# Kernel optimization log

Hardware: AMD Instinct MI355X
Metric: run time of the kernel (lower is better)

Reference implementation:

```python
import jax, jax.numpy as jnp
import numpy as np

V, E, H, M, C = 50000, 300, 256, 512, 20  # vocab, emb_dim, hid_dim, max_dim, n_classes
S, B = 512, 64  # seq_len, batch


def setup_inputs() -> dict:
    key = jax.random.key(0)
    ks = jax.random.split(key, 16)
    s = lambda i, shape: jax.random.normal(ks[i], shape, dtype=jnp.float32) * 0.05
    return dict(
        inp=jax.random.randint(ks[0], (S, B), 0, V),
        emb_table=s(1, (V, E)),
        c_l0=s(2, (H,)), c_r0=s(3, (H,)),
        W_l_w=s(4, (H, H)), W_l_b=s(5, (H,)),
        W_r_w=s(6, (H, H)), W_r_b=s(7, (H,)),
        W_sl_w=s(8, (H, E)), W_sl_b=s(9, (H,)),
        W_sr_w=s(10, (H, E)), W_sr_b=s(11, (H,)),
        max_w=s(12, (M, 2 * H + E)), max_b=s(13, (M,)),
        doc_w=s(14, (C, M)), doc_b=s(15, (C,)),
    )


def reference(inp, emb_table, c_l0, c_r0, W_l_w, W_l_b, W_r_w, W_r_b,
              W_sl_w, W_sl_b, W_sr_w, W_sr_b, max_w, max_b, doc_w, doc_b):
    emb = emb_table[inp]  # [S, B, E]
    # precomputed per-token projections (batched once, as in the original)
    emb_ls = jnp.einsum('sbe,he->sbh', emb, W_sl_w) + W_sl_b  # [S, B, H]
    emb_rs = jnp.einsum('sbe,he->sbh', emb, W_sr_w) + W_sr_b  # [S, B, H]

    batch = inp.shape[1]

    def make_step(W, b):
        def step(c, x):  # c: [B, H], x: [B, H]
            c = jnp.tanh(c @ W.T + b + x)
            return c, c
        return step

    c0_l = jnp.broadcast_to(c_l0, (batch, c_l0.shape[0]))
    c0_r = jnp.broadcast_to(c_r0, (batch, c_r0.shape[0]))
    _, c_ls = jax.lax.scan(make_step(W_l_w, W_l_b), c0_l, emb_ls)          # left-to-right
    _, c_rs = jax.lax.scan(make_step(W_r_w, W_r_b), c0_r, emb_rs[::-1])    # right-to-left
    c_rs = c_rs[::-1]  # re-align to original time order (stack(c_rs[::-1]))

    cat = jnp.concatenate([c_ls, emb, c_rs], axis=-1)  # [S, B, 2H+E]
    y = jnp.tanh(jnp.einsum('sbc,mc->sbm', cat, max_w) + max_b)  # [S, B, M]
    y_max = jnp.max(y, axis=0)  # [B, M] element-wise max-pool over time
    return jax.nn.log_softmax(y_max @ doc_w.T + doc_b, axis=-1)  # [B, C]
```

## Files before the change

### kernel.cpp

```cpp
#include <hip/hip_runtime.h>
#include <hip/hip_bf16.h>

constexpr int kS = 512;
constexpr int kB = 64;
constexpr int kE = 300;
constexpr int kH = 256;
constexpr int kM = 512;
constexpr int kC = 20;

typedef short s16x8 __attribute__((ext_vector_type(8)));
typedef float f32x4 __attribute__((ext_vector_type(4)));
typedef unsigned short u16x4 __attribute__((ext_vector_type(4)));
typedef _Float16 f16x8 __attribute__((ext_vector_type(8)));

__device__ __forceinline__ float fast_tanh(float z) {
    z = fminf(15.f, fmaxf(-15.f, z));
    float e = __expf(2.f * z);
    return 1.f - 2.f / (e + 1.f);
}

__device__ __forceinline__ unsigned short f2bf(float f) {
    __hip_bfloat16 h = __float2bfloat16(f);
    return *(unsigned short*)&h;
}
__device__ __forceinline__ float bf2f(unsigned short u) {
    __hip_bfloat16 h = *(__hip_bfloat16*)&u;
    return __bfloat162float(h);
}
union F16U { _Float16 h; unsigned short u; };
__device__ __forceinline__ unsigned short f16bits(_Float16 h) { F16U x; x.h = h; return x.u; }


__global__ __launch_bounds__(256) void prepw_kernel(
    const float* __restrict__ max_w,
    const float* __restrict__ wsl, const float* __restrict__ wsr,
    const float* __restrict__ wl, const float* __restrict__ wr,
    unsigned short* __restrict__ Wmax, unsigned short* __restrict__ Wproj,
    unsigned short* __restrict__ Wscan)
{
    int idx = blockIdx.x * 256 + threadIdx.x;
    if (idx < 512 * 832) {
        int r = idx / 832, c = idx - r * 832;
        float v;
        if (c < 556)      v = max_w[r * 812 + c];
        else if (c < 576) v = 0.f;
        else              v = max_w[r * 812 + (c - 20)];
        Wmax[idx] = f2bf(v);
    }
    if (idx < 512 * 320) {
        int r = idx / 320, c = idx - r * 320;
        float v = 0.f;
        if (c < 300) v = (r < 256) ? wsl[r * 300 + c] : wsr[(r - 256) * 300 + c];
        Wproj[idx] = f2bf(v);
    }
    if (idx < 2 * 256 * 256) {
        int d = idx >> 16, rc = idx & 65535;
        float v = (d ? wr : wl)[rc];
        Wscan[idx] = f16bits((_Float16)v);
    }
}

__global__ __launch_bounds__(128) void gather_kernel(
    const int* __restrict__ inp, const float* __restrict__ emb_table,
    unsigned short* __restrict__ E)
{
    const int row = blockIdx.x;
    const int b = row >> 9, s = row & 511;
    const int t = threadIdx.x;
    unsigned short* dst = E + (size_t)row * 320;
    const int v = inp[s * kB + b];
    const float* src = emb_table + (size_t)v * kE;
    if (t < 75) {
        float4 f = *(const float4*)&src[t * 4];
        u16x4 o = { f2bf(f.x), f2bf(f.y), f2bf(f.z), f2bf(f.w) };
        *(u16x4*)&dst[t * 4] = o;
    } else if (t < 80) {
        u16x4 z = { 0, 0, 0, 0 };
        *(u16x4*)&dst[300 + (t - 75) * 4] = z;
    }
}

__global__ __launch_bounds__(256) void proj_mfma_kernel(
    const unsigned short* __restrict__ E,
    const unsigned short* __restrict__ Wproj,
    const float* __restrict__ b_sl, const float* __restrict__ b_sr,
    unsigned short* __restrict__ XCL, unsigned short* __restrict__ XCR)
{
    __shared__ unsigned short As[128 * 40];
    __shared__ unsigned short Bs[128 * 40];
    const int tid = threadIdx.x;
    const int row0 = blockIdx.x * 128;
    const int col0 = blockIdx.y * 128;
    const int lane = tid & 63;
    const int wave = tid >> 6;
    const int wr = (wave >> 1) * 64, wc = (wave & 1) * 64;
    const int l15 = lane & 15, lk = (lane >> 4) * 8;
    const int srow = tid >> 1;
    const int sh = (tid & 1) * 16;

    const unsigned short* Ag = E + (size_t)(row0 + srow) * 320 + sh;
    const unsigned short* Bg = Wproj + (size_t)(col0 + srow) * 320 + sh;

    f32x4 acc[4][4] = {};
    float4 av0 = *(const float4*)Ag;
    float4 av1 = *(const float4*)(Ag + 8);
    float4 bv0 = *(const float4*)Bg;
    float4 bv1 = *(const float4*)(Bg + 8);

    for (int kk = 0; kk < 10; ++kk) {
        __syncthreads();
        *(float4*)&As[srow * 40 + sh] = av0;
        *(float4*)&As[srow * 40 + sh + 8] = av1;
        *(float4*)&Bs[srow * 40 + sh] = bv0;
        *(float4*)&Bs[srow * 40 + sh + 8] = bv1;
        __syncthreads();
        if (kk < 9) {
            av0 = *(const float4*)(Ag + (kk + 1) * 32);
            av1 = *(const float4*)(Ag + (kk + 1) * 32 + 8);
            bv0 = *(const float4*)(Bg + (kk + 1) * 32);
            bv1 = *(const float4*)(Bg + (kk + 1) * 32 + 8);
        }
        s16x8 af[4], bf[4];
#pragma unroll
        for (int f = 0; f < 4; ++f) {
            af[f] = *(const s16x8*)&As[(wr + f * 16 + l15) * 40 + lk];
            bf[f] = *(const s16x8*)&Bs[(wc + f * 16 + l15) * 40 + lk];
        }
#pragma unroll
        for (int i = 0; i < 4; ++i)
#pragma unroll
            for (int j = 0; j < 4; ++j)
                acc[i][j] = __builtin_amdgcn_mfma_f32_16x16x32_bf16(af[i], bf[j], acc[i][j], 0, 0, 0);
    }

    const int rbase = row0 + wr + (lane >> 4) * 4;
#pragma unroll
    for (int j = 0; j < 4; ++j) {
        const int col = col0 + wc + j * 16 + l15;
        const float bias = (col < kH) ? b_sl[col] : b_sr[col - kH];
        unsigned short* X = (col < kH) ? XCL : XCR;
        const int ccol = col & 255;
#pragma unroll
        for (int i = 0; i < 4; ++i) {
#pragma unroll
            for (int r = 0; r < 4; ++r) {
                const int row = rbase + i * 16 + r;
                const int s = row & 511, b = row >> 9;
                X[((size_t)s * 64 + b) * 256 + ccol] = f2bf(acc[i][j][r] + bias);
            }
        }
    }
}

__global__ __launch_bounds__(512, 2) void scan_mfma_kernel(
    const float* __restrict__ c_l0, const float* __restrict__ c_r0,
    const float* __restrict__ b_l, const float* __restrict__ b_r,
    const unsigned short* __restrict__ Wscan,
    unsigned short* __restrict__ XCL, unsigned short* __restrict__ XCR)
{
    __shared__ unsigned short cF[2][16 * 256];

    const int dir = blockIdx.x >> 2;
    const int bg  = blockIdx.x & 3;
    const int tid = threadIdx.x;
    const int lane = tid & 63;
    const int wave = tid >> 6;
    const int l15 = lane & 15;
    const int q4  = lane >> 4;
    const int lk  = q4 * 8;
    const int n0  = wave * 32;

    const float* bias = dir ? b_r : b_l;
    const float* c0v  = dir ? c_r0 : c_l0;
    const unsigned short* W = Wscan + (dir << 16);
    unsigned short* XC = dir ? XCR : XCL;

    f16x8 wf[2][8];
#pragma unroll
    for (int j = 0; j < 2; ++j)
#pragma unroll
        for (int ks = 0; ks < 8; ++ks)
            wf[j][ks] = *(const f16x8*)&W[(n0 + j * 16 + l15) * 256 + ks * 32 + lk];

    float biasv[2];
#pragma unroll
    for (int j = 0; j < 2; ++j) biasv[j] = bias[n0 + j * 16 + l15];

    unsigned short* xbase[4];
#pragma unroll
    for (int r = 0; r < 4; ++r)
        xbase[r] = XC + (size_t)(bg * 16 + q4 * 4 + r) * 256 + n0 + l15;

    int ridx[8], widx[2][4];
#pragma unroll
    for (int ks = 0; ks < 8; ++ks)
        ridx[ks] = (l15 * 256 + ks * 32 + lk) ^ ((l15 & 7) << 3);
#pragma unroll
    for (int j = 0; j < 2; ++j)
#pragma unroll
        for (int r = 0; r < 4; ++r) {
            int row = q4 * 4 + r;
            widx[j][r] = (row * 256 + n0 + j * 16 + l15) ^ ((row & 7) << 3);
        }

    if (tid < 256) {
        unsigned short hb = f16bits((_Float16)c0v[tid]);
        for (int row = 0; row < 16; ++row)
            cF[0][(row * 256 + tid) ^ ((row & 7) << 3)] = hb;
    }

    const int s0i = dir ? 511 : 0;
    const int s1i = dir ? 510 : 1;
    unsigned short xa[8], xb[8];
#pragma unroll
    for (int j = 0; j < 2; ++j)
#pragma unroll
        for (int r = 0; r < 4; ++r) {
            xa[j * 4 + r] = xbase[r][(size_t)s0i * 16384 + j * 16];
            xb[j * 4 + r] = xbase[r][(size_t)s1i * 16384 + j * 16];
        }
    __syncthreads();

    auto body = [&](int t, unsigned short (&xc)[8]) {
        const int st = dir ? (511 - t) : t;
        int sld = dir ? (st - 2) : (st + 2);
        sld = min(511, max(0, sld));
        const int p = t & 1;

        f32x4 acc[2];
#pragma unroll
        for (int j = 0; j < 2; ++j)
#pragma unroll
            for (int r = 0; r < 4; ++r)
                acc[j][r] = biasv[j] + bf2f(xc[j * 4 + r]);

#pragma unroll
        for (int j = 0; j < 2; ++j)
#pragma unroll
            for (int r = 0; r < 4; ++r)
                xc[j * 4 + r] = xbase[r][(size_t)sld * 16384 + j * 16];

        f16x8 ah[8];
#pragma unroll
        for (int ks = 0; ks < 8; ++ks)
            ah[ks] = *(const f16x8*)&cF[p][ridx[ks]];
#pragma unroll
        for (int ks = 0; ks < 8; ++ks) {
            acc[0] = __builtin_amdgcn_mfma_f32_16x16x32_f16(ah[ks], wf[0][ks], acc[0], 0, 0, 0);
            acc[1] = __builtin_amdgcn_mfma_f32_16x16x32_f16(ah[ks], wf[1][ks], acc[1], 0, 0, 0);
        }

#pragma unroll
        for (int j = 0; j < 2; ++j)
#pragma unroll
            for (int r = 0; r < 4; ++r) {
                float c = fast_tanh(acc[j][r]);
                xbase[r][(size_t)st * 16384 + j * 16] = f2bf(c);
                cF[p ^ 1][widx[j][r]] = f16bits((_Float16)c);
            }
        __syncthreads();
    };

    for (int t = 0; t < kS; t += 2) {
        body(t, xa);
        body(t + 1, xb);
    }
}

__global__ __launch_bounds__(256) void maxlayer_mfma_kernel(
    const unsigned short* __restrict__ XCL, const unsigned short* __restrict__ E,
    const unsigned short* __restrict__ XCR, const unsigned short* __restrict__ Wmax,
    float* __restrict__ part_max)
{
    __shared__ unsigned short As[128 * 40];
    __shared__ unsigned short Bs[128 * 40];
    __shared__ float red[2][128];
    const int tid = threadIdx.x;
    const int mt = blockIdx.x, sc = blockIdx.y, b = blockIdx.z;
    const int col0 = mt * 128;
    const int lane = tid & 63;
    const int wave = tid >> 6;
    const int wrow = wave >> 1;
    const int wr = wrow * 64, wc = (wave & 1) * 64;
    const int l15 = lane & 15, lk = (lane >> 4) * 8;
    const int srow = tid >> 1;
    const int sh = (tid & 1) * 16;

    const int s = sc * 128 + srow;
    const unsigned short* baseL = XCL + ((size_t)s * 64 + b) * 256 + sh;
    const unsigned short* baseE = E + (size_t)(b * 512 + s) * 320 + sh;
    const unsigned short* baseR = XCR + ((size_t)s * 64 + b) * 256 + sh;
    const unsigned short* Bg = Wmax + (size_t)(col0 + srow) * 832 + sh;

    auto aptr = [&](int kk) -> const unsigned short* {
        if (kk < 8)  return baseL + kk * 32;
        if (kk < 18) return baseE + (kk - 8) * 32;
        return baseR + (kk - 18) * 32;
    };

    f32x4 acc[4][4] = {};
    float4 av0 = *(const float4*)aptr(0);
    float4 av1 = *(const float4*)(aptr(0) + 8);
    float4 bv0 = *(const float4*)Bg;
    float4 bv1 = *(const float4*)(Bg + 8);

    for (int kk = 0; kk < 26; ++kk) {
        __syncthreads();
        *(float4*)&As[srow * 40 + sh] = av0;
        *(float4*)&As[srow * 40 + sh + 8] = av1;
        *(float4*)&Bs[srow * 40 + sh] = bv0;
        *(float4*)&Bs[srow * 40 + sh + 8] = bv1;
        __syncthreads();
        if (kk < 25) {
            const unsigned short* ap = aptr(kk + 1);
            av0 = *(const float4*)ap;
            av1 = *(const float4*)(ap + 8);
            bv0 = *(const float4*)(Bg + (kk + 1) * 32);
            bv1 = *(const float4*)(Bg + (kk + 1) * 32 + 8);
        }
        s16x8 af[4], bf[4];
#pragma unroll
        for (int f = 0; f < 4; ++f) {
            af[f] = *(const s16x8*)&As[(wr + f * 16 + l15) * 40 + lk];
            bf[f] = *(const s16x8*)&Bs[(wc + f * 16 + l15) * 40 + lk];
        }
#pragma unroll
        for (int i = 0; i < 4; ++i)
#pragma unroll
            for (int j = 0; j < 4; ++j)
                acc[i][j] = __builtin_amdgcn_mfma_f32_16x16x32_bf16(af[i], bf[j], acc[i][j], 0, 0, 0);
    }

#pragma unroll
    for (int j = 0; j < 4; ++j) {
        float m = -1e30f;
#pragma unroll
        for (int i = 0; i < 4; ++i)
#pragma unroll
            for (int r = 0; r < 4; ++r) m = fmaxf(m, acc[i][j][r]);
        m = fmaxf(m, __shfl_xor(m, 16));
        m = fmaxf(m, __shfl_xor(m, 32));
        if (lane < 16) red[wrow][wc + j * 16 + lane] = m;
    }
    __syncthreads();
    if (tid < 128) {
        float v = fmaxf(red[0][tid], red[1][tid]);
        part_max[((size_t)(b * 4 + sc)) * kM + col0 + tid] = v;
    }
}

__global__ __launch_bounds__(256) void final_kernel(
    const float* __restrict__ part_max, const float* __restrict__ max_b,
    const float* __restrict__ doc_w, const float* __restrict__ doc_b,
    float* __restrict__ out)
{
    const int b = blockIdx.x;
    const int t = threadIdx.x;
    __shared__ float ym[kM];
    __shared__ float red[160];
    __shared__ float logits[kC];

    for (int m = t; m < kM; m += 256) {
        float v = -1e30f;
        for (int ch = 0; ch < 4; ++ch)
            v = fmaxf(v, part_max[((size_t)(b * 4 + ch)) * kM + m]);
        ym[m] = fast_tanh(v + max_b[m]);
    }
    __syncthreads();
    if (t < 160) {
        int c = t >> 3, kg = t & 7;
        float s = 0.f;
        const float* wr = doc_w + c * kM + kg * 64;
        const float* yr = ym + kg * 64;
        for (int k = 0; k < 64; ++k) s += yr[k] * wr[k];
        red[t] = s;
    }
    __syncthreads();
    if (t < kC) {
        float s = doc_b[t];
        for (int kg = 0; kg < 8; ++kg) s += red[t * 8 + kg];
        logits[t] = s;
    }
    __syncthreads();
    if (t == 0) {
        float mx = logits[0];
        for (int c = 1; c < kC; ++c) mx = fmaxf(mx, logits[c]);
        float se = 0.f;
        for (int c = 0; c < kC; ++c) se += __expf(logits[c] - mx);
        float lse = mx + __logf(se);
        for (int c = 0; c < kC; ++c) out[b * kC + c] = logits[c] - lse;
    }
}

extern "C" void kernel_launch(void* const* d_in, const int* in_sizes, int n_in,
                              void* d_out, int out_size, void* d_ws, size_t ws_size,
                              hipStream_t stream) {
    const int* inp = (const int*)d_in[0];
    const float* emb_table = (const float*)d_in[1];
    const float* c_l0 = (const float*)d_in[2];
    const float* c_r0 = (const float*)d_in[3];
    const float* W_l_w = (const float*)d_in[4];
    const float* W_l_b = (const float*)d_in[5];
    const float* W_r_w = (const float*)d_in[6];
    const float* W_r_b = (const float*)d_in[7];
    const float* W_sl_w = (const float*)d_in[8];
    const float* W_sl_b = (const float*)d_in[9];
    const float* W_sr_w = (const float*)d_in[10];
    const float* W_sr_b = (const float*)d_in[11];
    const float* max_w = (const float*)d_in[12];
    const float* max_b = (const float*)d_in[13];
    const float* doc_w = (const float*)d_in[14];
    const float* doc_b = (const float*)d_in[15];
    float* out = (float*)d_out;

    char* w = (char*)d_ws;
    unsigned short* E     = (unsigned short*)(w);
    unsigned short* XCL   = (unsigned short*)(w + 20971520);
    unsigned short* XCR   = (unsigned short*)(w + 37748736);
    unsigned short* Wmax  = (unsigned short*)(w + 54525952);
    unsigned short* Wproj = (unsigned short*)(w + 55377920);
    float* part_max       = (float*)(w + 55705600);
    unsigned short* Wscan = (unsigned short*)(w + 56229888);

    prepw_kernel<<<(512 * 832 + 255) / 256, 256, 0, stream>>>(
        max_w, W_sl_w, W_sr_w, W_l_w, W_r_w, Wmax, Wproj, Wscan);
    gather_kernel<<<kS * kB, 128, 0, stream>>>(inp, emb_table, E);
    proj_mfma_kernel<<<dim3(256, 4), 256, 0, stream>>>(
        E, Wproj, W_sl_b, W_sr_b, XCL, XCR);
    scan_mfma_kernel<<<8, 512, 0, stream>>>(
        c_l0, c_r0, W_l_b, W_r_b, Wscan, XCL, XCR);
    maxlayer_mfma_kernel<<<dim3(4, 4, 64), 256, 0, stream>>>(
        XCL, E, XCR, Wmax, part_max);
    final_kernel<<<kB, 256, 0, stream>>>(part_max, max_b, doc_w, doc_b, out);
}
```

Baseline: 629.5 us.

## Transpose scan MFMA operands for packed stores and split accumulation chains

Swaps the A/B operands of the scan recurrence MFMA so each lane holds four consecutive hidden units. Global x loads and bf16 stores then become 8-byte vectorized accesses, and the LDS state write becomes a packed f16x4 store. The K loop is split into two independent accumulator chains to shorten the MFMA dependency latency on the serial critical path. Tanh now uses raw exp2/rcp intrinsics with packed conversions but without clamping, and the f16 conversion switches to round-toward-zero, which slightly changes numerics.

Measured after the change: 519.1 us. 1.21x faster.

```diff
diff --git a/kernel.cpp b/kernel.cpp
--- a/kernel.cpp
+++ b/kernel.cpp
@@ -12,6 +12,7 @@
 typedef float f32x4 __attribute__((ext_vector_type(4)));
 typedef unsigned short u16x4 __attribute__((ext_vector_type(4)));
 typedef _Float16 f16x8 __attribute__((ext_vector_type(8)));
+typedef __fp16 hf16x2 __attribute__((ext_vector_type(2)));
 
 __device__ __forceinline__ float fast_tanh(float z) {
     z = fminf(15.f, fmaxf(-15.f, z));
@@ -22,10 +23,6 @@
 __device__ __forceinline__ unsigned short f2bf(float f) {
     __hip_bfloat16 h = __float2bfloat16(f);
     return *(unsigned short*)&h;
-}
-__device__ __forceinline__ float bf2f(unsigned short u) {
-    __hip_bfloat16 h = *(__hip_bfloat16*)&u;
-    return __bfloat162float(h);
 }
 union F16U { _Float16 h; unsigned short u; };
 __device__ __forceinline__ unsigned short f16bits(_Float16 h) { F16U x; x.h = h; return x.u; }
@@ -167,7 +164,6 @@
     const int wave = tid >> 6;
     const int l15 = lane & 15;
     const int q4  = lane >> 4;
-    const int lk  = q4 * 8;
     const int n0  = wave * 32;
 
     const float* bias = dir ? b_r : b_l;
@@ -180,28 +176,24 @@
     for (int j = 0; j < 2; ++j)
 #pragma unroll
         for (int ks = 0; ks < 8; ++ks)
-            wf[j][ks] = *(const f16x8*)&W[(n0 + j * 16 + l15) * 256 + ks * 32 + lk];
-
-    float biasv[2];
-#pragma unroll
-    for (int j = 0; j < 2; ++j) biasv[j] = bias[n0 + j * 16 + l15];
-
-    unsigned short* xbase[4];
-#pragma unroll
-    for (int r = 0; r < 4; ++r)
-        xbase[r] = XC + (size_t)(bg * 16 + q4 * 4 + r) * 256 + n0 + l15;
-
-    int ridx[8], widx[2][4];
+            wf[j][ks] = *(const f16x8*)&W[(n0 + j * 16 + l15) * 256 + ks * 32 + q4 * 8];
+
+    float biasv[2][4];
+#pragma unroll
+    for (int j = 0; j < 2; ++j)
+#pragma unroll
+        for (int r = 0; r < 4; ++r)
+            biasv[j][r] = bias[n0 + j * 16 + q4 * 4 + r];
+
+    const unsigned int base0 = (unsigned)((bg * 16 + l15) * 256 + n0 + q4 * 4);
+
+    int ridx[8], widx[2];
 #pragma unroll
     for (int ks = 0; ks < 8; ++ks)
-        ridx[ks] = (l15 * 256 + ks * 32 + lk) ^ ((l15 & 7) << 3);
+        ridx[ks] = (l15 * 256 + ks * 32 + q4 * 8) ^ ((l15 & 7) << 3);
 #pragma unroll
     for (int j = 0; j < 2; ++j)
-#pragma unroll
-        for (int r = 0; r < 4; ++r) {
-            int row = q4 * 4 + r;
-            widx[j][r] = (row * 256 + n0 + j * 16 + l15) ^ ((row & 7) << 3);
-        }
+        widx[j] = (l15 * 256 + n0 + j * 16 + q4 * 4) ^ ((l15 & 7) << 3);
 
     if (tid < 256) {
         unsigned short hb = f16bits((_Float16)c0v[tid]);
@@ -211,53 +203,75 @@
 
     const int s0i = dir ? 511 : 0;
     const int s1i = dir ? 510 : 1;
-    unsigned short xa[8], xb[8];
-#pragma unroll
-    for (int j = 0; j < 2; ++j)
-#pragma unroll
-        for (int r = 0; r < 4; ++r) {
-            xa[j * 4 + r] = xbase[r][(size_t)s0i * 16384 + j * 16];
-            xb[j * 4 + r] = xbase[r][(size_t)s1i * 16384 + j * 16];
-        }
+    uint2 xa[2], xb[2];
+#pragma unroll
+    for (int j = 0; j < 2; ++j) {
+        xa[j] = *(const uint2*)(XC + base0 + (unsigned)s0i * 16384u + j * 16);
+        xb[j] = *(const uint2*)(XC + base0 + (unsigned)s1i * 16384u + j * 16);
+    }
     __syncthreads();
 
-    auto body = [&](int t, unsigned short (&xc)[8]) {
+    auto body = [&](int t, uint2 (&xc)[2]) {
         const int st = dir ? (511 - t) : t;
-        int sld = dir ? (st - 2) : (st + 2);
-        sld = min(511, max(0, sld));
+        const int sld = dir ? (st - 2 < 0 ? 0 : st - 2)
+                            : (st + 2 > 511 ? 511 : st + 2);
         const int p = t & 1;
 
-        f32x4 acc[2];
+        f32x4 acc[2], acc2[2];
+#pragma unroll
+        for (int j = 0; j < 2; ++j) {
+            const unsigned d0 = xc[j].x, d1 = xc[j].y;
+            acc[j][0] = biasv[j][0]; acc[j][1] = biasv[j][1];
+            acc[j][2] = biasv[j][2]; acc[j][3] = biasv[j][3];
+            acc2[j][0] = __uint_as_float(d0 << 16);
+            acc2[j][1] = __uint_as_float(d0 & 0xffff0000u);
+            acc2[j][2] = __uint_as_float(d1 << 16);
+            acc2[j][3] = __uint_as_float(d1 & 0xffff0000u);
+        }
+
 #pragma unroll
         for (int j = 0; j < 2; ++j)
-#pragma unroll
-            for (int r = 0; r < 4; ++r)
-                acc[j][r] = biasv[j] + bf2f(xc[j * 4 + r]);
-
-#pragma unroll
-        for (int j = 0; j < 2; ++j)
-#pragma unroll
-            for (int r = 0; r < 4; ++r)
-                xc[j * 4 + r] = xbase[r][(size_t)sld * 16384 + j * 16];
+            xc[j] = *(const uint2*)(XC + base0 + (unsigned)sld * 16384u + j * 16);
 
         f16x8 ah[8];
 #pragma unroll
         for (int ks = 0; ks < 8; ++ks)
             ah[ks] = *(const f16x8*)&cF[p][ridx[ks]];
 #pragma unroll
-        for (int ks = 0; ks < 8; ++ks) {
-            acc[0] = __builtin_amdgcn_mfma_f32_16x16x32_f16(ah[ks], wf[0][ks], acc[0], 0, 0, 0);
-            acc[1] = __builtin_amdgcn_mfma_f32_16x16x32_f16(ah[ks], wf[1][ks], acc[1], 0, 0, 0);
-        }
-
-#pragma unroll
-        for (int j = 0; j < 2; ++j)
-#pragma unroll
-            for (int r = 0; r < 4; ++r) {
-                float c = fast_tanh(acc[j][r]);
-                xbase[r][(size_t)st * 16384 + j * 16] = f2bf(c);
-                cF[p ^ 1][widx[j][r]] = f16bits((_Float16)c);
+        for (int ks = 0; ks < 4; ++ks) {
+            acc[0]  = __builtin_amdgcn_mfma_f32_16x16x32_f16(wf[0][ks],     ah[ks],     acc[0],  0, 0, 0);
+            acc[1]  = __builtin_amdgcn_mfma_f32_16x16x32_f16(wf[1][ks],     ah[ks],     acc[1],  0, 0, 0);
+            acc2[0] = __builtin_amdgcn_mfma_f32_16x16x32_f16(wf[0][ks + 4], ah[ks + 4], acc2[0], 0, 0, 0);
+            acc2[1] = __builtin_amdgcn_mfma_f32_16x16x32_f16(wf[1][ks + 4], ah[ks + 4], acc2[1], 0, 0, 0);
+        }
+
+#pragma unroll
+        for (int j = 0; j < 2; ++j) {
+            float t0, t1, t2, t3;
+            {
+                float z0 = acc[j][0] + acc2[j][0];
+                float z1 = acc[j][1] + acc2[j][1];
+                float z2 = acc[j][2] + acc2[j][2];
+                float z3 = acc[j][3] + acc2[j][3];
+                float e0 = __builtin_amdgcn_exp2f(z0 * 2.8853900817779268f);
+                float e1 = __builtin_amdgcn_exp2f(z1 * 2.8853900817779268f);
+                float e2 = __builtin_amdgcn_exp2f(z2 * 2.8853900817779268f);
+                float e3 = __builtin_amdgcn_exp2f(z3 * 2.8853900817779268f);
+                t0 = fmaf(-2.f, __builtin_amdgcn_rcpf(e0 + 1.f), 1.f);
+                t1 = fmaf(-2.f, __builtin_amdgcn_rcpf(e1 + 1.f), 1.f);
+                t2 = fmaf(-2.f, __builtin_amdgcn_rcpf(e2 + 1.f), 1.f);
+                t3 = fmaf(-2.f, __builtin_amdgcn_rcpf(e3 + 1.f), 1.f);
             }
+            uint2 pkb;
+            asm("v_cvt_pk_bf16_f32 %0, %1, %2" : "=v"(pkb.x) : "v"(t0), "v"(t1));
+            asm("v_cvt_pk_bf16_f32 %0, %1, %2" : "=v"(pkb.y) : "v"(t2), "v"(t3));
+            *(uint2*)(XC + base0 + (unsigned)st * 16384u + j * 16) = pkb;
+            union { hf16x2 h; unsigned u; } h0, h1;
+            h0.h = __builtin_amdgcn_cvt_pkrtz(t0, t1);
+            h1.h = __builtin_amdgcn_cvt_pkrtz(t2, t3);
+            uint2 hw; hw.x = h0.u; hw.y = h1.u;
+            *(uint2*)&cF[p ^ 1][widx[j]] = hw;
+        }
         __syncthreads();
     };
 
```
